# Performance work log

Hardware: AMD Instinct MI355X
Metric: run time of the kernel (lower is better)

The kernel has to match this reference:

```python
import jax, jax.numpy as jnp
import numpy as np

# Integration setup: torch code integrates t in [0,1] with dopri5.
# We use the dopri5 (RK45) Butcher tableau with a fixed step count so the
# reference is deterministic and jit/vjp friendly; per-stage math is identical.
N_STEPS = 16
T0, T1 = 0.0, 1.0

# dopri5 tableau
C2, C3, C4, C5, C6 = 1/5, 3/10, 4/5, 8/9, 1.0
A21 = 1/5
A31, A32 = 3/40, 9/40
A41, A42, A43 = 44/45, -56/15, 32/9
A51, A52, A53, A54 = 19372/6561, -25360/2187, 64448/6561, -212/729
A61, A62, A63, A64, A65 = 9017/3168, -355/33, 46732/5247, 49/176, -5103/18656
B1, B3, B4, B5, B6 = 35/384, 500/1113, 125/192, -2187/6784, 11/84  # 5th-order weights (b2=b7=0)


def setup_inputs() -> dict:
    key = jax.random.key(0)
    k0, k1, k2, k3 = jax.random.split(key, 4)
    B, D, H = 16384, 256, 512
    x = jax.random.normal(k0, (B, D), jnp.float32)
    W1 = jax.random.normal(k1, (D, H), jnp.float32) / np.sqrt(D).astype(np.float32)
    b1 = jnp.zeros((H,), jnp.float32)
    W2 = jax.random.normal(k2, (H, D), jnp.float32) / np.sqrt(H).astype(np.float32)
    b2 = jnp.zeros((D,), jnp.float32)
    Wfc = jax.random.normal(k3, (D, 1), jnp.float32) / np.sqrt(D).astype(np.float32)
    bfc = jnp.zeros((1,), jnp.float32)
    return {"x": x, "W1": W1, "b1": b1, "W2": W2, "b2": b2, "Wfc": Wfc, "bfc": bfc}


def reference(x, W1, b1, W2, b2, Wfc, bfc):
    def f(t, y):  # autonomous MLP vector field: dim -> hidden -> dim
        return jnp.tanh(y @ W1 + b1) @ W2 + b2

    dt = jnp.float32((T1 - T0) / N_STEPS)

    def step(carry, _):
        t, y = carry
        k1 = f(t, y)
        k2 = f(t + C2 * dt, y + dt * (A21 * k1))
        k3 = f(t + C3 * dt, y + dt * (A31 * k1 + A32 * k2))
        k4 = f(t + C4 * dt, y + dt * (A41 * k1 + A42 * k2 + A43 * k3))
        k5 = f(t + C5 * dt, y + dt * (A51 * k1 + A52 * k2 + A53 * k3 + A54 * k4))
        k6 = f(t + C6 * dt, y + dt * (A61 * k1 + A62 * k2 + A63 * k3 + A64 * k4 + A65 * k5))
        y_next = y + dt * (B1 * k1 + B3 * k3 + B4 * k4 + B5 * k5 + B6 * k6)
        return (t + dt, y_next), None

    (_, y1), _ = jax.lax.scan(step, (jnp.float32(T0), x), None, length=N_STEPS)
    return y1 @ Wfc + bfc  # [B, 1]
```

## Files before the change

kernel.cpp:

```cpp
#include <hip/hip_runtime.h>

typedef unsigned short u16;
typedef unsigned int   u32;
typedef __bf16 bf16x8 __attribute__((ext_vector_type(8)));
typedef float  f32x4  __attribute__((ext_vector_type(4)));
typedef u32    u32x2  __attribute__((ext_vector_type(2)));

#define DIMD  256
#define DIMH  512
#define MTILE 64
#define NTHREADS 512

#define USTR 264
#define HSTR 520
#define U_BASE 0
#define H_BASE (MTILE*USTR)
#define LDS_U16 (H_BASE + MTILE*HSTR)

#define DT 0.0625f

__device__ __forceinline__ u16 f2bf(float f) {
  u32 u = __float_as_uint(f);
  u += 0x7FFFu + ((u >> 16) & 1u);
  return (u16)(u >> 16);
}
__device__ __forceinline__ u32 pk(float a, float b) {
  return (u32)f2bf(a) | ((u32)f2bf(b) << 16);
}
__device__ __forceinline__ float bflo(u32 p) { return __uint_as_float(p << 16); }
__device__ __forceinline__ float bfhi(u32 p) { return __uint_as_float(p & 0xFFFF0000u); }
__device__ __forceinline__ float tanh_fast(float x) {
  float e = __builtin_amdgcn_exp2f(x * 2.8853900817779268f);
  return 1.0f - 2.0f * __builtin_amdgcn_rcpf(e + 1.0f);
}

__global__ void convert_w(const float* __restrict__ W1, const float* __restrict__ W2,
                          u16* __restrict__ w1t, u16* __restrict__ w2t) {
  int idx = blockIdx.x * 256 + threadIdx.x;
  {
    int n = idx >> 8, k = idx & 255;
    w1t[idx] = f2bf(W1[k * DIMH + n]);
  }
  {
    int n = idx >> 9, k = idx & 511;
    w2t[idx] = f2bf(W2[k * DIMD + n]);
  }
}

__global__ __attribute__((amdgpu_flat_work_group_size(NTHREADS, NTHREADS),
                          amdgpu_waves_per_eu(2, 2)))
void ode_fused(
    const float* __restrict__ x,   const float* __restrict__ b1,
    const float* __restrict__ b2,  const float* __restrict__ wfc,
    const float* __restrict__ bfc, const u16* __restrict__ w1t,
    const u16* __restrict__ w2t,   float* __restrict__ out)
{
  __shared__ u16 lds[LDS_U16];

  const int tid   = threadIdx.x;
  const int wg    = blockIdx.x;
  const int wv    = tid >> 6;
  const int lane  = tid & 63;
  const int lanel = lane & 15;
  const int laneq = lane >> 4;


  u32 b1p[8], b2p[4];
#pragma unroll
  for (int mb = 0; mb < 4; ++mb) {
    int base = wv * 64 + mb * 16 + laneq * 4;
    b1p[mb * 2 + 0] = pk(b1[base + 0], b1[base + 1]);
    b1p[mb * 2 + 1] = pk(b1[base + 2], b1[base + 3]);
  }
#pragma unroll
  for (int mb = 0; mb < 2; ++mb) {
    int base = wv * 32 + mb * 16 + laneq * 4;
    b2p[mb * 2 + 0] = pk(b2[base + 0], b2[base + 1]);
    b2p[mb * 2 + 1] = pk(b2[base + 2], b2[base + 3]);
  }

  float yv[32];
#pragma unroll
  for (int nb = 0; nb < 4; ++nb)
#pragma unroll
    for (int mb = 0; mb < 2; ++mb) {
      const float4 v = *(const float4*)&x[(wg * 64 + nb * 16 + lanel) * DIMD +
                                          wv * 32 + mb * 16 + laneq * 4];
      int i = nb * 8 + mb * 4;
      yv[i + 0] = v.x; yv[i + 1] = v.y; yv[i + 2] = v.z; yv[i + 3] = v.w;
    }

#pragma unroll
  for (int nb = 0; nb < 4; ++nb)
#pragma unroll
    for (int mb = 0; mb < 2; ++mb) {
      int i = nb * 8 + mb * 4;
      u32x2 w; w.x = pk(yv[i], yv[i + 1]); w.y = pk(yv[i + 2], yv[i + 3]);
      *(u32x2*)&lds[U_BASE + (nb * 16 + lanel) * USTR + wv * 32 + mb * 16 + laneq * 4] = w;
    }
  __syncthreads();

  const u16* w1base[4];
#pragma unroll
  for (int mb = 0; mb < 4; ++mb)
    w1base[mb] = w1t + (wv * 64 + mb * 16 + lanel) * DIMD + laneq * 8;
  const u16* w2base[2];
#pragma unroll
  for (int mb = 0; mb < 2; ++mb)
    w2base[mb] = w2t + (wv * 32 + mb * 16 + lanel) * DIMH + laneq * 8;

  u32 st[48];

#pragma unroll 1
  for (int step = 0; step < 16; ++step) {
#pragma unroll 1
    for (int s = 1; s <= 6; ++s) {
      f32x4 acc[4][4];
#pragma unroll
      for (int mb = 0; mb < 4; ++mb)
#pragma unroll
        for (int nb = 0; nb < 4; ++nb) acc[mb][nb] = (f32x4){0.f, 0.f, 0.f, 0.f};
#pragma unroll 1
      for (int kk = 0; kk < 8; ++kk) {
        bf16x8 a[4], bu[4];
#pragma unroll
        for (int mb = 0; mb < 4; ++mb)
          a[mb] = *(const bf16x8*)(w1base[mb] + kk * 32);
#pragma unroll
        for (int nb = 0; nb < 4; ++nb)
          bu[nb] = *(const bf16x8*)&lds[U_BASE + (nb * 16 + lanel) * USTR + kk * 32 + laneq * 8];
#pragma unroll
        for (int mb = 0; mb < 4; ++mb)
#pragma unroll
          for (int nb = 0; nb < 4; ++nb)
            acc[mb][nb] = __builtin_amdgcn_mfma_f32_16x16x32_bf16(a[mb], bu[nb], acc[mb][nb], 0, 0, 0);
      }
#pragma unroll
      for (int mb = 0; mb < 4; ++mb)
#pragma unroll
        for (int nb = 0; nb < 4; ++nb) {
          float h0 = tanh_fast(acc[mb][nb][0] + bflo(b1p[mb * 2 + 0]));
          float h1 = tanh_fast(acc[mb][nb][1] + bfhi(b1p[mb * 2 + 0]));
          float h2 = tanh_fast(acc[mb][nb][2] + bflo(b1p[mb * 2 + 1]));
          float h3 = tanh_fast(acc[mb][nb][3] + bfhi(b1p[mb * 2 + 1]));
          u32x2 w; w.x = pk(h0, h1); w.y = pk(h2, h3);
          *(u32x2*)&lds[H_BASE + (nb * 16 + lanel) * HSTR + wv * 64 + mb * 16 + laneq * 4] = w;
        }
      __syncthreads();

      f32x4 acc2[2][4];
#pragma unroll
      for (int mb = 0; mb < 2; ++mb)
#pragma unroll
        for (int nb = 0; nb < 4; ++nb) acc2[mb][nb] = (f32x4){0.f, 0.f, 0.f, 0.f};
#pragma unroll 1
      for (int kk = 0; kk < 16; ++kk) {
        bf16x8 a2[2], bh[4];
#pragma unroll
        for (int mb = 0; mb < 2; ++mb)
          a2[mb] = *(const bf16x8*)(w2base[mb] + kk * 32);
#pragma unroll
        for (int nb = 0; nb < 4; ++nb)
          bh[nb] = *(const bf16x8*)&lds[H_BASE + (nb * 16 + lanel) * HSTR + kk * 32 + laneq * 8];
#pragma unroll
        for (int mb = 0; mb < 2; ++mb)
#pragma unroll
          for (int nb = 0; nb < 4; ++nb)
            acc2[mb][nb] = __builtin_amdgcn_mfma_f32_16x16x32_bf16(a2[mb], bh[nb], acc2[mb][nb], 0, 0, 0);
      }

      if (s == 1) {
        const float C = DT * 0.2f;
#pragma unroll
        for (int mb = 0; mb < 2; ++mb)
#pragma unroll
          for (int nb = 0; nb < 4; ++nb) {
            int i = nb * 8 + mb * 4, p = nb * 4 + mb * 2;
            float k0 = acc2[mb][nb][0] + bflo(b2p[mb * 2 + 0]);
            float k1 = acc2[mb][nb][1] + bfhi(b2p[mb * 2 + 0]);
            float k2 = acc2[mb][nb][2] + bflo(b2p[mb * 2 + 1]);
            float k3 = acc2[mb][nb][3] + bfhi(b2p[mb * 2 + 1]);
            st[p] = pk(k0, k1); st[p + 1] = pk(k2, k3);
            u32x2 w;
            w.x = pk(yv[i] + C * k0, yv[i + 1] + C * k1);
            w.y = pk(yv[i + 2] + C * k2, yv[i + 3] + C * k3);
            *(u32x2*)&lds[U_BASE + (nb * 16 + lanel) * USTR + wv * 32 + mb * 16 + laneq * 4] = w;
          }
      } else if (s == 2) {
        const float C1 = DT * 0.075f, C2 = DT * 0.225f;
#pragma unroll
        for (int mb = 0; mb < 2; ++mb)
#pragma unroll
          for (int nb = 0; nb < 4; ++nb) {
            int i = nb * 8 + mb * 4, p = nb * 4 + mb * 2;
            float k0 = acc2[mb][nb][0] + bflo(b2p[mb * 2 + 0]);
            float k1 = acc2[mb][nb][1] + bfhi(b2p[mb * 2 + 0]);
            float k2 = acc2[mb][nb][2] + bflo(b2p[mb * 2 + 1]);
            float k3 = acc2[mb][nb][3] + bfhi(b2p[mb * 2 + 1]);
            st[16 + p] = pk(k0, k1); st[16 + p + 1] = pk(k2, k3);
            u32x2 w;
            w.x = pk(yv[i]     + C1 * bflo(st[p])     + C2 * k0,
                     yv[i + 1] + C1 * bfhi(st[p])     + C2 * k1);
            w.y = pk(yv[i + 2] + C1 * bflo(st[p + 1]) + C2 * k2,
                     yv[i + 3] + C1 * bfhi(st[p + 1]) + C2 * k3);
            *(u32x2*)&lds[U_BASE + (nb * 16 + lanel) * USTR + wv * 32 + mb * 16 + laneq * 4] = w;
          }
      } else if (s == 3) {
        const float C1 = DT * (float)(44.0/45.0);
        const float C2 = DT * (float)(-56.0/15.0);
        const float C3 = DT * (float)(32.0/9.0);
#pragma unroll
        for (int mb = 0; mb < 2; ++mb)
#pragma unroll
          for (int nb = 0; nb < 4; ++nb) {
            int i = nb * 8 + mb * 4, p = nb * 4 + mb * 2;
            float k0 = acc2[mb][nb][0] + bflo(b2p[mb * 2 + 0]);
            float k1 = acc2[mb][nb][1] + bfhi(b2p[mb * 2 + 0]);
            float k2 = acc2[mb][nb][2] + bflo(b2p[mb * 2 + 1]);
            float k3 = acc2[mb][nb][3] + bfhi(b2p[mb * 2 + 1]);
            st[32 + p] = pk(k0, k1); st[32 + p + 1] = pk(k2, k3);
            u32x2 w;
            w.x = pk(yv[i]     + C1 * bflo(st[p])     + C2 * bflo(st[16 + p])     + C3 * k0,
                     yv[i + 1] + C1 * bfhi(st[p])     + C2 * bfhi(st[16 + p])     + C3 * k1);
            w.y = pk(yv[i + 2] + C1 * bflo(st[p + 1]) + C2 * bflo(st[16 + p + 1]) + C3 * k2,
                     yv[i + 3] + C1 * bfhi(st[p + 1]) + C2 * bfhi(st[16 + p + 1]) + C3 * k3);
            *(u32x2*)&lds[U_BASE + (nb * 16 + lanel) * USTR + wv * 32 + mb * 16 + laneq * 4] = w;
          }
      } else if (s == 4) {
        const float C51 = DT * (float)(19372.0/6561.0);
        const float C52 = DT * (float)(-25360.0/2187.0);
        const float C53 = DT * (float)(64448.0/6561.0);
        const float C54 = DT * (float)(-212.0/729.0);
        const float D61 = DT * (float)(9017.0/3168.0  - 35.0/384.0);
        const float D62 = DT * (float)(-355.0/33.0);
        const float D63 = DT * (float)(46732.0/5247.0 - 500.0/1113.0);
        const float D64 = DT * (float)(49.0/176.0     - 125.0/192.0);
        const float E1  = DT * (float)(35.0/384.0);
        const float E3  = DT * (float)(500.0/1113.0);
        const float E4  = DT * (float)(125.0/192.0);
#pragma unroll
        for (int mb = 0; mb < 2; ++mb)
#pragma unroll
          for (int nb = 0; nb < 4; ++nb) {
            int i = nb * 8 + mb * 4, p = nb * 4 + mb * 2;
            float k40 = acc2[mb][nb][0] + bflo(b2p[mb * 2 + 0]);
            float k41 = acc2[mb][nb][1] + bfhi(b2p[mb * 2 + 0]);
            float k42 = acc2[mb][nb][2] + bflo(b2p[mb * 2 + 1]);
            float k43 = acc2[mb][nb][3] + bfhi(b2p[mb * 2 + 1]);
            float k10 = bflo(st[p]),      k11 = bfhi(st[p]);
            float k12 = bflo(st[p + 1]),  k13 = bfhi(st[p + 1]);
            float k20 = bflo(st[16 + p]), k21 = bfhi(st[16 + p]);
            float k22 = bflo(st[16 + p + 1]), k23 = bfhi(st[16 + p + 1]);
            float k30 = bflo(st[32 + p]), k31 = bfhi(st[32 + p]);
            float k32 = bflo(st[32 + p + 1]), k33 = bfhi(st[32 + p + 1]);
            u32x2 w;
            w.x = pk(yv[i]     + C51 * k10 + C52 * k20 + C53 * k30 + C54 * k40,
                     yv[i + 1] + C51 * k11 + C52 * k21 + C53 * k31 + C54 * k41);
            w.y = pk(yv[i + 2] + C51 * k12 + C52 * k22 + C53 * k32 + C54 * k42,
                     yv[i + 3] + C51 * k13 + C52 * k23 + C53 * k33 + C54 * k43);
            *(u32x2*)&lds[U_BASE + (nb * 16 + lanel) * USTR + wv * 32 + mb * 16 + laneq * 4] = w;
            st[p]     = pk(D61 * k10 + D62 * k20 + D63 * k30 + D64 * k40,
                           D61 * k11 + D62 * k21 + D63 * k31 + D64 * k41);
            st[p + 1] = pk(D61 * k12 + D62 * k22 + D63 * k32 + D64 * k42,
                           D61 * k13 + D62 * k23 + D63 * k33 + D64 * k43);
            yv[i]     += E1 * k10 + E3 * k30 + E4 * k40;
            yv[i + 1] += E1 * k11 + E3 * k31 + E4 * k41;
            yv[i + 2] += E1 * k12 + E3 * k32 + E4 * k42;
            yv[i + 3] += E1 * k13 + E3 * k33 + E4 * k43;
          }
      } else if (s == 5) {
        const float D65 = DT * (float)(-5103.0/18656.0 + 2187.0/6784.0);
        const float E5  = DT * (float)(-2187.0/6784.0);
#pragma unroll
        for (int mb = 0; mb < 2; ++mb)
#pragma unroll
          for (int nb = 0; nb < 4; ++nb) {
            int i = nb * 8 + mb * 4, p = nb * 4 + mb * 2;
            float k0 = acc2[mb][nb][0] + bflo(b2p[mb * 2 + 0]);
            float k1 = acc2[mb][nb][1] + bfhi(b2p[mb * 2 + 0]);
            float k2 = acc2[mb][nb][2] + bflo(b2p[mb * 2 + 1]);
            float k3 = acc2[mb][nb][3] + bfhi(b2p[mb * 2 + 1]);
            u32x2 w;
            w.x = pk(yv[i]     + bflo(st[p])     + D65 * k0,
                     yv[i + 1] + bfhi(st[p])     + D65 * k1);
            w.y = pk(yv[i + 2] + bflo(st[p + 1]) + D65 * k2,
                     yv[i + 3] + bfhi(st[p + 1]) + D65 * k3);
            *(u32x2*)&lds[U_BASE + (nb * 16 + lanel) * USTR + wv * 32 + mb * 16 + laneq * 4] = w;
            yv[i]     += E5 * k0;
            yv[i + 1] += E5 * k1;
            yv[i + 2] += E5 * k2;
            yv[i + 3] += E5 * k3;
          }
      } else {
        const float E6 = DT * (float)(11.0/84.0);
#pragma unroll
        for (int mb = 0; mb < 2; ++mb)
#pragma unroll
          for (int nb = 0; nb < 4; ++nb) {
            int i = nb * 8 + mb * 4;
            yv[i]     += E6 * (acc2[mb][nb][0] + bflo(b2p[mb * 2 + 0]));
            yv[i + 1] += E6 * (acc2[mb][nb][1] + bfhi(b2p[mb * 2 + 0]));
            yv[i + 2] += E6 * (acc2[mb][nb][2] + bflo(b2p[mb * 2 + 1]));
            yv[i + 3] += E6 * (acc2[mb][nb][3] + bfhi(b2p[mb * 2 + 1]));
            u32x2 w;
            w.x = pk(yv[i], yv[i + 1]); w.y = pk(yv[i + 2], yv[i + 3]);
            *(u32x2*)&lds[U_BASE + (nb * 16 + lanel) * USTR + wv * 32 + mb * 16 + laneq * 4] = w;
          }
      }
      __syncthreads();
    }
  }

  {
    float wfcv[8];
#pragma unroll
    for (int mb = 0; mb < 2; ++mb)
#pragma unroll
      for (int r = 0; r < 4; ++r)
        wfcv[mb * 4 + r] = wfc[wv * 32 + mb * 16 + laneq * 4 + r];
    float* redf = (float*)lds;
    float pr[4];
#pragma unroll
    for (int nb = 0; nb < 4; ++nb) {
      float p = 0.f;
#pragma unroll
      for (int mb = 0; mb < 2; ++mb)
#pragma unroll
        for (int r = 0; r < 4; ++r)
          p += yv[nb * 8 + mb * 4 + r] * wfcv[mb * 4 + r];
      p += __shfl_xor(p, 16);
      p += __shfl_xor(p, 32);
      pr[nb] = p;
    }
    if (laneq == 0) {
#pragma unroll
      for (int nb = 0; nb < 4; ++nb)
        redf[(nb * 16 + lanel) * 8 + wv] = pr[nb];
    }
    __syncthreads();
    if (tid < 64) {
      float s = bfc[0];
#pragma unroll
      for (int w = 0; w < 8; ++w) s += redf[tid * 8 + w];
      out[wg * 64 + tid] = s;
    }
  }
}

extern "C" void kernel_launch(void* const* d_in, const int* in_sizes, int n_in,
                              void* d_out, int out_size, void* d_ws, size_t ws_size,
                              hipStream_t stream) {
  const float* x   = (const float*)d_in[0];
  const float* W1  = (const float*)d_in[1];
  const float* b1  = (const float*)d_in[2];
  const float* W2  = (const float*)d_in[3];
  const float* b2  = (const float*)d_in[4];
  const float* wfc = (const float*)d_in[5];
  const float* bfc = (const float*)d_in[6];
  float* out = (float*)d_out;

  u16* w1t = (u16*)d_ws;
  u16* w2t = w1t + DIMH * DIMD;

  hipLaunchKernelGGL(convert_w, dim3(512), dim3(256), 0, stream, W1, W2, w1t, w2t);
  hipLaunchKernelGGL(ode_fused, dim3(16384 / MTILE), dim3(NTHREADS), 0, stream,
                     x, b1, b2, wfc, bfc, w1t, w2t, out);
}
```

Baseline: 1.814 ms.

## Double-buffer MFMA operand loads, spill k2 to LDS, use hardware bf16 pack and LDS-only barriers

Both GEMM inner loops now use a two-deep software pipeline: the next k-slice's weight and LDS operands are loaded while the MFMAs for the current slice issue. The first slice of the next GEMM's weights is prefetched across the tanh and RK-update phases. The k2 stage values move from registers to a new LDS buffer, cutting the st array from 48 to 32 registers to relieve register pressure under the 2-waves constraint. __syncthreads is replaced by a barrier that waits only on LDS counters, and bf16 packing uses the hardware cvt_pk builtin when it is available. The risks are a larger LDS footprint and the hardware conversion rounding slightly differently from the manual version.

```diff
diff --git a/kernel.cpp b/kernel.cpp
--- a/kernel.cpp
+++ b/kernel.cpp
@@ -25,13 +25,25 @@
   return (u16)(u >> 16);
 }
 __device__ __forceinline__ u32 pk(float a, float b) {
+#if __has_builtin(__builtin_amdgcn_cvt_pk_bf16_f32)
+  auto v = __builtin_amdgcn_cvt_pk_bf16_f32(a, b);
+  u32 r; __builtin_memcpy(&r, &v, 4); return r;
+#else
   return (u32)f2bf(a) | ((u32)f2bf(b) << 16);
+#endif
 }
 __device__ __forceinline__ float bflo(u32 p) { return __uint_as_float(p << 16); }
 __device__ __forceinline__ float bfhi(u32 p) { return __uint_as_float(p & 0xFFFF0000u); }
 __device__ __forceinline__ float tanh_fast(float x) {
   float e = __builtin_amdgcn_exp2f(x * 2.8853900817779268f);
   return 1.0f - 2.0f * __builtin_amdgcn_rcpf(e + 1.0f);
+}
+
+__device__ __forceinline__ void bar_lds() {
+  asm volatile("" ::: "memory");
+  __builtin_amdgcn_s_waitcnt(0xC07F);
+  __builtin_amdgcn_s_barrier();
+  asm volatile("" ::: "memory");
 }
 
 __global__ void convert_w(const float* __restrict__ W1, const float* __restrict__ W2,
@@ -45,6 +57,23 @@
     int n = idx >> 9, k = idx & 511;
     w2t[idx] = f2bf(W2[k * DIMD + n]);
   }
+}
+
+__device__ __forceinline__ void mfma_16(f32x4 (&acc)[4][4],
+                                        const bf16x8 (&a)[4], const bf16x8 (&b)[4]) {
+#pragma unroll
+  for (int mb = 0; mb < 4; ++mb)
+#pragma unroll
+    for (int nb = 0; nb < 4; ++nb)
+      acc[mb][nb] = __builtin_amdgcn_mfma_f32_16x16x32_bf16(a[mb], b[nb], acc[mb][nb], 0, 0, 0);
+}
+__device__ __forceinline__ void mfma_8(f32x4 (&acc)[2][4],
+                                       const bf16x8 (&a)[2], const bf16x8 (&b)[4]) {
+#pragma unroll
+  for (int mb = 0; mb < 2; ++mb)
+#pragma unroll
+    for (int nb = 0; nb < 4; ++nb)
+      acc[mb][nb] = __builtin_amdgcn_mfma_f32_16x16x32_bf16(a[mb], b[nb], acc[mb][nb], 0, 0, 0);
 }
 
 __global__ __attribute__((amdgpu_flat_work_group_size(NTHREADS, NTHREADS),
@@ -56,6 +85,7 @@
     const u16* __restrict__ w2t,   float* __restrict__ out)
 {
   __shared__ u16 lds[LDS_U16];
+  __shared__ u32 k2f[16 * NTHREADS];
 
   const int tid   = threadIdx.x;
   const int wg    = blockIdx.x;
@@ -64,6 +94,11 @@
   const int lanel = lane & 15;
   const int laneq = lane >> 4;
 
+  const u16* uRd = &lds[U_BASE + lanel * USTR + laneq * 8];
+  const u16* hRd = &lds[H_BASE + lanel * HSTR + laneq * 8];
+  u16* uWr = &lds[U_BASE + lanel * USTR + wv * 32 + laneq * 4];
+  u16* hWr = &lds[H_BASE + lanel * HSTR + wv * 64 + laneq * 4];
+
 
   u32 b1p[8], b2p[4];
 #pragma unroll
@@ -96,9 +131,8 @@
     for (int mb = 0; mb < 2; ++mb) {
       int i = nb * 8 + mb * 4;
       u32x2 w; w.x = pk(yv[i], yv[i + 1]); w.y = pk(yv[i + 2], yv[i + 3]);
-      *(u32x2*)&lds[U_BASE + (nb * 16 + lanel) * USTR + wv * 32 + mb * 16 + laneq * 4] = w;
-    }
-  __syncthreads();
+      *(u32x2*)(uWr + nb * 16 * USTR + mb * 16) = w;
+    }
 
   const u16* w1base[4];
 #pragma unroll
@@ -109,7 +143,28 @@
   for (int mb = 0; mb < 2; ++mb)
     w2base[mb] = w2t + (wv * 32 + mb * 16 + lanel) * DIMH + laneq * 8;
 
-  u32 st[48];
+  auto ldA1 = [&](bf16x8 (&a)[4], int kk) {
+#pragma unroll
+    for (int mb = 0; mb < 4; ++mb) a[mb] = *(const bf16x8*)(w1base[mb] + kk * 32);
+  };
+  auto ldB1 = [&](bf16x8 (&b)[4], int kk) {
+#pragma unroll
+    for (int nb = 0; nb < 4; ++nb) b[nb] = *(const bf16x8*)(uRd + nb * 16 * USTR + kk * 32);
+  };
+  auto ldA2 = [&](bf16x8 (&a)[2], int kk) {
+#pragma unroll
+    for (int mb = 0; mb < 2; ++mb) a[mb] = *(const bf16x8*)(w2base[mb] + kk * 32);
+  };
+  auto ldB2 = [&](bf16x8 (&b)[4], int kk) {
+#pragma unroll
+    for (int nb = 0; nb < 4; ++nb) b[nb] = *(const bf16x8*)(hRd + nb * 16 * HSTR + kk * 32);
+  };
+
+  u32 st[32];
+
+  bf16x8 aP1[4];
+  ldA1(aP1, 0);
+  bar_lds();
 
 #pragma unroll 1
   for (int step = 0; step < 16; ++step) {
@@ -120,21 +175,23 @@
       for (int mb = 0; mb < 4; ++mb)
 #pragma unroll
         for (int nb = 0; nb < 4; ++nb) acc[mb][nb] = (f32x4){0.f, 0.f, 0.f, 0.f};
+      bf16x8 aA[4], bA[4], aB[4], bB[4];
+#pragma unroll
+      for (int mb = 0; mb < 4; ++mb) aA[mb] = aP1[mb];
+      ldB1(bA, 0);
 #pragma unroll 1
-      for (int kk = 0; kk < 8; ++kk) {
-        bf16x8 a[4], bu[4];
-#pragma unroll
-        for (int mb = 0; mb < 4; ++mb)
-          a[mb] = *(const bf16x8*)(w1base[mb] + kk * 32);
-#pragma unroll
-        for (int nb = 0; nb < 4; ++nb)
-          bu[nb] = *(const bf16x8*)&lds[U_BASE + (nb * 16 + lanel) * USTR + kk * 32 + laneq * 8];
-#pragma unroll
-        for (int mb = 0; mb < 4; ++mb)
-#pragma unroll
-          for (int nb = 0; nb < 4; ++nb)
-            acc[mb][nb] = __builtin_amdgcn_mfma_f32_16x16x32_bf16(a[mb], bu[nb], acc[mb][nb], 0, 0, 0);
+      for (int kk2 = 0; kk2 < 3; ++kk2) {
+        ldA1(aB, 2 * kk2 + 1); ldB1(bB, 2 * kk2 + 1);
+        mfma_16(acc, aA, bA);
+        ldA1(aA, 2 * kk2 + 2); ldB1(bA, 2 * kk2 + 2);
+        mfma_16(acc, aB, bB);
       }
+      ldA1(aB, 7); ldB1(bB, 7);
+      mfma_16(acc, aA, bA);
+      bf16x8 aP2[2];
+      ldA2(aP2, 0);
+      mfma_16(acc, aB, bB);
+
 #pragma unroll
       for (int mb = 0; mb < 4; ++mb)
 #pragma unroll
@@ -144,30 +201,30 @@
           float h2 = tanh_fast(acc[mb][nb][2] + bflo(b1p[mb * 2 + 1]));
           float h3 = tanh_fast(acc[mb][nb][3] + bfhi(b1p[mb * 2 + 1]));
           u32x2 w; w.x = pk(h0, h1); w.y = pk(h2, h3);
-          *(u32x2*)&lds[H_BASE + (nb * 16 + lanel) * HSTR + wv * 64 + mb * 16 + laneq * 4] = w;
+          *(u32x2*)(hWr + nb * 16 * HSTR + mb * 16) = w;
         }
-      __syncthreads();
+      bar_lds();
 
       f32x4 acc2[2][4];
 #pragma unroll
       for (int mb = 0; mb < 2; ++mb)
 #pragma unroll
         for (int nb = 0; nb < 4; ++nb) acc2[mb][nb] = (f32x4){0.f, 0.f, 0.f, 0.f};
+      bf16x8 cA[2], dA[4], cB[2], dB[4];
+#pragma unroll
+      for (int mb = 0; mb < 2; ++mb) cA[mb] = aP2[mb];
+      ldB2(dA, 0);
 #pragma unroll 1
-      for (int kk = 0; kk < 16; ++kk) {
-        bf16x8 a2[2], bh[4];
-#pragma unroll
-        for (int mb = 0; mb < 2; ++mb)
-          a2[mb] = *(const bf16x8*)(w2base[mb] + kk * 32);
-#pragma unroll
-        for (int nb = 0; nb < 4; ++nb)
-          bh[nb] = *(const bf16x8*)&lds[H_BASE + (nb * 16 + lanel) * HSTR + kk * 32 + laneq * 8];
-#pragma unroll
-        for (int mb = 0; mb < 2; ++mb)
-#pragma unroll
-          for (int nb = 0; nb < 4; ++nb)
-            acc2[mb][nb] = __builtin_amdgcn_mfma_f32_16x16x32_bf16(a2[mb], bh[nb], acc2[mb][nb], 0, 0, 0);
+      for (int kk2 = 0; kk2 < 7; ++kk2) {
+        ldA2(cB, 2 * kk2 + 1); ldB2(dB, 2 * kk2 + 1);
+        mfma_8(acc2, cA, dA);
+        ldA2(cA, 2 * kk2 + 2); ldB2(dA, 2 * kk2 + 2);
+        mfma_8(acc2, cB, dB);
       }
+      ldA2(cB, 15); ldB2(dB, 15);
+      mfma_8(acc2, cA, dA);
+      ldA1(aP1, 0);
+      mfma_8(acc2, cB, dB);
 
       if (s == 1) {
         const float C = DT * 0.2f;
@@ -184,10 +241,32 @@
             u32x2 w;
             w.x = pk(yv[i] + C * k0, yv[i + 1] + C * k1);
             w.y = pk(yv[i + 2] + C * k2, yv[i + 3] + C * k3);
-            *(u32x2*)&lds[U_BASE + (nb * 16 + lanel) * USTR + wv * 32 + mb * 16 + laneq * 4] = w;
+            *(u32x2*)(uWr + nb * 16 * USTR + mb * 16) = w;
           }
       } else if (s == 2) {
         const float C1 = DT * 0.075f, C2 = DT * 0.225f;
+#pragma unroll
+        for (int mb = 0; mb < 2; ++mb)
+#pragma unroll
+          for (int nb = 0; nb < 4; ++nb) {
+            int i = nb * 8 + mb * 4, p = nb * 4 + mb * 2;
+            float k0 = acc2[mb][nb][0] + bflo(b2p[mb * 2 + 0]);
+            float k1 = acc2[mb][nb][1] + bfhi(b2p[mb * 2 + 0]);
+            float k2 = acc2[mb][nb][2] + bflo(b2p[mb * 2 + 1]);
+            float k3 = acc2[mb][nb][3] + bfhi(b2p[mb * 2 + 1]);
+            k2f[p * NTHREADS + tid]       = pk(k0, k1);
+            k2f[(p + 1) * NTHREADS + tid] = pk(k2, k3);
+            u32x2 w;
+            w.x = pk(yv[i]     + C1 * bflo(st[p])     + C2 * k0,
+                     yv[i + 1] + C1 * bfhi(st[p])     + C2 * k1);
+            w.y = pk(yv[i + 2] + C1 * bflo(st[p + 1]) + C2 * k2,
+                     yv[i + 3] + C1 * bfhi(st[p + 1]) + C2 * k3);
+            *(u32x2*)(uWr + nb * 16 * USTR + mb * 16) = w;
+          }
+      } else if (s == 3) {
+        const float C1 = DT * (float)(44.0/45.0);
+        const float C2 = DT * (float)(-56.0/15.0);
+        const float C3 = DT * (float)(32.0/9.0);
 #pragma unroll
         for (int mb = 0; mb < 2; ++mb)
 #pragma unroll
@@ -198,33 +277,13 @@
             float k2 = acc2[mb][nb][2] + bflo(b2p[mb * 2 + 1]);
             float k3 = acc2[mb][nb][3] + bfhi(b2p[mb * 2 + 1]);
             st[16 + p] = pk(k0, k1); st[16 + p + 1] = pk(k2, k3);
-            u32x2 w;
-            w.x = pk(yv[i]     + C1 * bflo(st[p])     + C2 * k0,
-                     yv[i + 1] + C1 * bfhi(st[p])     + C2 * k1);
-            w.y = pk(yv[i + 2] + C1 * bflo(st[p + 1]) + C2 * k2,
-                     yv[i + 3] + C1 * bfhi(st[p + 1]) + C2 * k3);
-            *(u32x2*)&lds[U_BASE + (nb * 16 + lanel) * USTR + wv * 32 + mb * 16 + laneq * 4] = w;
-          }
-      } else if (s == 3) {
-        const float C1 = DT * (float)(44.0/45.0);
-        const float C2 = DT * (float)(-56.0/15.0);
-        const float C3 = DT * (float)(32.0/9.0);
-#pragma unroll
-        for (int mb = 0; mb < 2; ++mb)
-#pragma unroll
-          for (int nb = 0; nb < 4; ++nb) {
-            int i = nb * 8 + mb * 4, p = nb * 4 + mb * 2;
-            float k0 = acc2[mb][nb][0] + bflo(b2p[mb * 2 + 0]);
-            float k1 = acc2[mb][nb][1] + bfhi(b2p[mb * 2 + 0]);
-            float k2 = acc2[mb][nb][2] + bflo(b2p[mb * 2 + 1]);
-            float k3 = acc2[mb][nb][3] + bfhi(b2p[mb * 2 + 1]);
-            st[32 + p] = pk(k0, k1); st[32 + p + 1] = pk(k2, k3);
-            u32x2 w;
-            w.x = pk(yv[i]     + C1 * bflo(st[p])     + C2 * bflo(st[16 + p])     + C3 * k0,
-                     yv[i + 1] + C1 * bfhi(st[p])     + C2 * bfhi(st[16 + p])     + C3 * k1);
-            w.y = pk(yv[i + 2] + C1 * bflo(st[p + 1]) + C2 * bflo(st[16 + p + 1]) + C3 * k2,
-                     yv[i + 3] + C1 * bfhi(st[p + 1]) + C2 * bfhi(st[16 + p + 1]) + C3 * k3);
-            *(u32x2*)&lds[U_BASE + (nb * 16 + lanel) * USTR + wv * 32 + mb * 16 + laneq * 4] = w;
+            u32 q0 = k2f[p * NTHREADS + tid], q1 = k2f[(p + 1) * NTHREADS + tid];
+            u32x2 w;
+            w.x = pk(yv[i]     + C1 * bflo(st[p])     + C2 * bflo(q0) + C3 * k0,
+                     yv[i + 1] + C1 * bfhi(st[p])     + C2 * bfhi(q0) + C3 * k1);
+            w.y = pk(yv[i + 2] + C1 * bflo(st[p + 1]) + C2 * bflo(q1) + C3 * k2,
+                     yv[i + 3] + C1 * bfhi(st[p + 1]) + C2 * bfhi(q1) + C3 * k3);
+            *(u32x2*)(uWr + nb * 16 * USTR + mb * 16) = w;
           }
       } else if (s == 4) {
         const float C51 = DT * (float)(19372.0/6561.0);
@@ -249,16 +308,17 @@
             float k43 = acc2[mb][nb][3] + bfhi(b2p[mb * 2 + 1]);
             float k10 = bflo(st[p]),      k11 = bfhi(st[p]);
             float k12 = bflo(st[p + 1]),  k13 = bfhi(st[p + 1]);
-            float k20 = bflo(st[16 + p]), k21 = bfhi(st[16 + p]);
-            float k22 = bflo(st[16 + p + 1]), k23 = bfhi(st[16 + p + 1]);
-            float k30 = bflo(st[32 + p]), k31 = bfhi(st[32 + p]);
-            float k32 = bflo(st[32 + p + 1]), k33 = bfhi(st[32 + p + 1]);
+            u32 q0 = k2f[p * NTHREADS + tid], q1 = k2f[(p + 1) * NTHREADS + tid];
+            float k20 = bflo(q0), k21 = bfhi(q0);
+            float k22 = bflo(q1), k23 = bfhi(q1);
+            float k30 = bflo(st[16 + p]),     k31 = bfhi(st[16 + p]);
+            float k32 = bflo(st[16 + p + 1]), k33 = bfhi(st[16 + p + 1]);
             u32x2 w;
             w.x = pk(yv[i]     + C51 * k10 + C52 * k20 + C53 * k30 + C54 * k40,
                      yv[i + 1] + C51 * k11 + C52 * k21 + C53 * k31 + C54 * k41);
             w.y = pk(yv[i + 2] + C51 * k12 + C52 * k22 + C53 * k32 + C54 * k42,
                      yv[i + 3] + C51 * k13 + C52 * k23 + C53 * k33 + C54 * k43);
-            *(u32x2*)&lds[U_BASE + (nb * 16 + lanel) * USTR + wv * 32 + mb * 16 + laneq * 4] = w;
+            *(u32x2*)(uWr + nb * 16 * USTR + mb * 16) = w;
             st[p]     = pk(D61 * k10 + D62 * k20 + D63 * k30 + D64 * k40,
                            D61 * k11 + D62 * k21 + D63 * k31 + D64 * k41);
             st[p + 1] = pk(D61 * k12 + D62 * k22 + D63 * k32 + D64 * k42,
@@ -285,7 +345,7 @@
                      yv[i + 1] + bfhi(st[p])     + D65 * k1);
             w.y = pk(yv[i + 2] + bflo(st[p + 1]) + D65 * k2,
                      yv[i + 3] + bfhi(st[p + 1]) + D65 * k3);
-            *(u32x2*)&lds[U_BASE + (nb * 16 + lanel) * USTR + wv * 32 + mb * 16 + laneq * 4] = w;
+            *(u32x2*)(uWr + nb * 16 * USTR + mb * 16) = w;
             yv[i]     += E5 * k0;
             yv[i + 1] += E5 * k1;
             yv[i + 2] += E5 * k2;
@@ -304,10 +364,10 @@
             yv[i + 3] += E6 * (acc2[mb][nb][3] + bfhi(b2p[mb * 2 + 1]));
             u32x2 w;
             w.x = pk(yv[i], yv[i + 1]); w.y = pk(yv[i + 2], yv[i + 3]);
-            *(u32x2*)&lds[U_BASE + (nb * 16 + lanel) * USTR + wv * 32 + mb * 16 + laneq * 4] = w;
+            *(u32x2*)(uWr + nb * 16 * USTR + mb * 16) = w;
           }
       }
-      __syncthreads();
+      bar_lds();
     }
   }
 
```

Result: faster. 1.617 ms (-10.8%).
